# Performance work log

Hardware: AMD Instinct MI355X
Metric: run time of the kernel (lower is better)

The kernel has to match this reference:

```python
import jax, jax.numpy as jnp
import numpy as np

B, CIN, COUT, H, W = 16, 128, 128, 64, 64
E, PS, FF = 8, 16, 8
GC, HID, HC = 4 * FF, 64, COUT * 4  # gate_channel, gate hidden, bottleneck hidden


def conv(x, w, stride=1, pad=0, groups=1):
    # x: [B,C,H,W], w: [O,I/groups,kh,kw]
    return jax.lax.conv_general_dilated(
        x, w, (stride, stride), [(pad, pad), (pad, pad)], feature_group_count=groups)


def group_norm(x, scale, bias, groups, eps=1e-5):
    b, c = x.shape[:2]
    xr = x.reshape(b, groups, c // groups, *x.shape[2:])
    m = xr.mean(axis=(2, 3, 4), keepdims=True)
    v = xr.var(axis=(2, 3, 4), keepdims=True)
    xr = (xr - m) * jax.lax.rsqrt(v + eps)
    return xr.reshape(x.shape) * scale[None, :, None, None] + bias[None, :, None, None]


def setup_inputs() -> dict:
    key = jax.random.key(0)
    ks = jax.random.split(key, 8)
    f = lambda k, shp: jax.random.normal(k, shp, jnp.float32) * 0.05
    return dict(
        x=jax.random.normal(ks[0], (B, CIN, H, W), jnp.float32),
        w_exp=f(ks[1], (E, COUT, CIN, 3, 3)),
        gn_exp_s=jnp.ones((E, COUT), jnp.float32),
        gn_exp_b=jnp.zeros((E, COUT), jnp.float32),
        w1=f(ks[2], (GC, HID)), b1=jnp.zeros((HID,), jnp.float32),
        w2=f(ks[3], (HID, E)), b2=jnp.zeros((E,), jnp.float32),
        w_pw1=f(ks[4], (HC, COUT, 1, 1)),
        gn1_s=jnp.ones((HC,), jnp.float32), gn1_b=jnp.zeros((HC,), jnp.float32),
        w_dw=f(ks[5], (HC, 1, 3, 3)),
        gn2_s=jnp.ones((HC,), jnp.float32), gn2_b=jnp.zeros((HC,), jnp.float32),
        w_pw2=f(ks[6], (COUT, HC, 1, 1)),
        gn3_s=jnp.ones((COUT,), jnp.float32), gn3_b=jnp.zeros((COUT,), jnp.float32),
    )


def reference(x, w_exp, gn_exp_s, gn_exp_b, w1, b1, w2, b2,
              w_pw1, gn1_s, gn1_b, w_dw, gn2_s, gn2_b, w_pw2, gn3_s, gn3_b):
    # ---- Conv experts (residual 3x3 conv + GN + SiLU), vmapped over experts ----
    def expert(w, s, b):
        y = conv(x, w, pad=1)
        y = group_norm(y, s, b, groups=min(8, COUT))
        return jax.nn.silu(y) + x  # use_residual=True, CIN == COUT

    ys = jax.vmap(expert)(w_exp, gn_exp_s, gn_exp_b)  # [E,B,C,H,W]

    # ---- Router gate: Fourier features of patch-center coordinates ----
    ph, pw = H // PS, W // PS
    cy = (jnp.arange(ph, dtype=jnp.float32) + 0.5) / ph
    cx = (jnp.arange(pw, dtype=jnp.float32) + 0.5) / pw
    freqs = (2.0 ** jnp.arange(FF, dtype=jnp.float32)) * jnp.pi
    ay = cy[:, None] * freqs  # [ph,FF]
    ax = cx[:, None] * freqs  # [pw,FF]
    feats = jnp.concatenate([
        jnp.broadcast_to(jnp.sin(ay)[:, None, :], (ph, pw, FF)),
        jnp.broadcast_to(jnp.cos(ay)[:, None, :], (ph, pw, FF)),
        jnp.broadcast_to(jnp.sin(ax)[None, :, :], (ph, pw, FF)),
        jnp.broadcast_to(jnp.cos(ax)[None, :, :], (ph, pw, FF)),
    ], axis=-1)  # [ph,pw,4*FF] == gate_channel
    hgate = jax.nn.silu(feats @ w1 + b1)
    wts = jax.nn.softmax(hgate @ w2 + b2, axis=-1)  # [ph,pw,E]

    # ---- Patch-wise combine of expert outputs ----
    wmap = jnp.repeat(jnp.repeat(wts, PS, axis=0), PS, axis=1)  # [H,W,E]
    combined = jnp.einsum('ebchw,hwe->bchw', ys, wmap)

    # ---- Inverted bottleneck: 1x1 -> dw3x3 -> 1x1(stride2) with GN+SiLU ----
    h = jax.nn.silu(group_norm(conv(combined, w_pw1), gn1_s, gn1_b, groups=8))
    h = jax.nn.silu(group_norm(conv(h, w_dw, pad=1, groups=HC), gn2_s, gn2_b, groups=8))
    h = jax.nn.silu(group_norm(conv(h, w_pw2, stride=2), gn3_s, gn3_b, groups=8))
    return h  # [B, COUT, H//2, W//2]
```

## Files before the change

kernel.cpp:

```cpp
#include <hip/hip_runtime.h>
#include <hip/hip_bf16.h>


#define B_ 16
#define CIN_ 128
#define COUT_ 128
#define H_ 64
#define W_ 64
#define HW_ 4096
#define E_ 8
#define FF_ 8
#define GC_ 32
#define HID_ 64
#define HC_ 512

typedef __hip_bfloat16 bf16;
typedef __bf16 bf16x8 __attribute__((ext_vector_type(8)));
typedef float f32x4 __attribute__((ext_vector_type(4)));
typedef float f32x16 __attribute__((ext_vector_type(16)));

__device__ __forceinline__ float siluf(float v) { return v / (1.f + __expf(-v)); }
__device__ __forceinline__ float bf2f(bf16 v) { return __bfloat162float(v); }
__device__ __forceinline__ bf16 f2bf(float v) { return __float2bfloat16(v); }

__device__ __forceinline__ void async16(void* lds, const void* g) {
  __builtin_amdgcn_global_load_lds(
      (const __attribute__((address_space(1))) unsigned int*)g,
      (__attribute__((address_space(3))) unsigned int*)lds, 16, 0, 0);
}

__global__ void gate_kernel(const float* __restrict__ w1, const float* __restrict__ b1,
                            const float* __restrict__ w2, const float* __restrict__ b2,
                            float* __restrict__ wts) {
  int p = threadIdx.x;
  if (p >= 16) return;
  int i = p >> 2, j = p & 3;
  float cy = (i + 0.5f) * 0.25f;
  float cx = (j + 0.5f) * 0.25f;
  float feats[GC_];
#pragma unroll
  for (int f = 0; f < FF_; ++f) {
    float fr = 3.14159265358979f * (float)(1 << f);
    float ay = cy * fr, ax = cx * fr;
    feats[f] = sinf(ay);
    feats[FF_ + f] = cosf(ay);
    feats[2 * FF_ + f] = sinf(ax);
    feats[3 * FF_ + f] = cosf(ax);
  }
  float hid[HID_];
  for (int k = 0; k < HID_; ++k) {
    float a = b1[k];
#pragma unroll
    for (int m = 0; m < GC_; ++m) a = fmaf(feats[m], w1[m * HID_ + k], a);
    hid[k] = siluf(a);
  }
  float lg[E_];
  float mx = -1e30f;
#pragma unroll
  for (int e = 0; e < E_; ++e) {
    float a = b2[e];
    for (int k = 0; k < HID_; ++k) a = fmaf(hid[k], w2[k * E_ + e], a);
    lg[e] = a;
    mx = fmaxf(mx, a);
  }
  float s = 0.f;
#pragma unroll
  for (int e = 0; e < E_; ++e) { lg[e] = __expf(lg[e] - mx); s += lg[e]; }
  float inv = 1.f / s;
#pragma unroll
  for (int e = 0; e < E_; ++e) wts[p * E_ + e] = lg[e] * inv;
}

__global__ __launch_bounds__(256) void xt_kernel(const float* __restrict__ x,
                                                 bf16* __restrict__ xT) {
  __shared__ float t[128][65];
  int b = blockIdx.x >> 6, h = blockIdx.x & 63;
  int tid = threadIdx.x;
  int w = tid & 63, c4 = tid >> 6;
  const float* xb = x + ((size_t)(b * 128) * 64 + h) * 64;
#pragma unroll 4
  for (int rep = 0; rep < 32; ++rep) {
    int ci = rep * 4 + c4;
    t[ci][w] = xb[(size_t)ci * HW_ + w];
  }
  __syncthreads();
  bf16* dst = xT + (size_t)(b * 64 + h) * 8192;
#pragma unroll 4
  for (int rep = 0; rep < 32; ++rep) {
    int o = rep * 256 + tid;
    int cg = o >> 9, w2 = (o >> 3) & 63, lo = o & 7;
    dst[o] = f2bf(t[cg * 8 + lo][w2]);
  }
}

__global__ void wt_kernel(const float* __restrict__ w_exp, bf16* __restrict__ wT) {
  int idx = blockIdx.x * 256 + threadIdx.x;
  if (idx >= 1179648) return;
  int lo = idx & 7;
  int co = (idx >> 3) & 127;
  int cg = (idx >> 10) & 15;
  int rest = idx >> 14;
  int tap = rest % 9, e = rest / 9;
  int ci = cg * 8 + lo;
  wT[idx] = f2bf(w_exp[(((size_t)(e * 128 + co) * 128 + ci) * 9) + tap]);
}

__global__ void wpT_kernel(const float* __restrict__ w_pw1, const float* __restrict__ w_pw2,
                           bf16* __restrict__ wp1T, bf16* __restrict__ wp2T) {
  int idx = blockIdx.x * 256 + threadIdx.x;
  if (idx < 65536) wp1T[idx] = f2bf(w_pw1[idx]);
  else if (idx < 131072) wp2T[idx - 65536] = f2bf(w_pw2[idx - 65536]);
}

__global__ __launch_bounds__(256, 2) void conv_mfma(
    const bf16* __restrict__ xT, const bf16* __restrict__ wT,
    float* __restrict__ statsE, bf16* __restrict__ ys) {
  __shared__ __align__(16) char xls[4 * 6336];
  __shared__ __align__(16) char wls[2][3 * 8192];
  __shared__ float red[4][8][2];

  int blk = blockIdx.x;
  int xcd = blk & 7;
  int r2 = blk >> 3;
  int b = xcd * 2 + (r2 & 1);
  int rest = r2 >> 1;
  int rt = rest & 15, e = rest >> 4;

  int tid = threadIdx.x, lane = tid & 63, wave = tid >> 6;
  int hi = lane >> 5, l31 = lane & 31;
  int h0 = rt * 4;

  if (tid < 48) {
    int cg = tid / 12, rem = tid % 12;
    int r = rem >> 1, edge = rem & 1;
    *(uint4*)(xls + cg * 6336 + r * 1056 + edge * 1040) = make_uint4(0u, 0u, 0u, 0u);
  }
  int rbad = (rt == 0) ? 0 : (rt == 15 ? 5 : -1);
  if (rbad >= 0) {
    int cg = tid >> 6, slot = (tid & 63) + 1;
    *(uint4*)(xls + cg * 6336 + rbad * 1056 + slot * 16) = make_uint4(0u, 0u, 0u, 0u);
  }

  f32x16 acc[4][2];
#pragma unroll
  for (int mt = 0; mt < 4; ++mt)
#pragma unroll
    for (int nt = 0; nt < 2; ++nt)
#pragma unroll
      for (int r = 0; r < 16; ++r) acc[mt][nt][r] = 0.f;

  for (int q = 0; q < 4; ++q) {
    if (q) __syncthreads();
    {
      int cg = wave;
#pragma unroll
      for (int r = 0; r < 6; ++r) {
        int h = h0 - 1 + r;
        if ((unsigned)h < 64u) {
          const char* g = (const char*)xT +
              ((size_t)((b * 64 + h) * 16) + q * 4 + cg) * 1024 + lane * 16;
          async16(xls + cg * 6336 + r * 1056 + 16, g);
        }
      }
    }
#pragma unroll
    for (int s = 0; s < 6; ++s) {
      int seg = wave * 6 + s;
      int tap = seg >> 3, rem = seg & 7;
      int cg = rem >> 1, cb = rem & 1;
      const char* g = (const char*)wT +
          ((size_t)(((e * 9 + tap) * 16) + q * 4 + cg) * 128 + cb * 64) * 16 + lane * 16;
      async16(wls[0] + (tap * 4 + cg) * 2048 + cb * 1024, g);
    }
    __syncthreads();

    for (int dr = 0; dr < 3; ++dr) {
      int buf = dr & 1;
      if (dr < 2) {
#pragma unroll
        for (int s = 0; s < 6; ++s) {
          int seg = wave * 6 + s;
          int tap = seg >> 3, rem = seg & 7;
          int cg = rem >> 1, cb = rem & 1;
          const char* g = (const char*)wT +
              ((size_t)(((e * 9 + (dr + 1) * 3 + tap) * 16) + q * 4 + cg) * 128 + cb * 64) * 16 +
              lane * 16;
          async16(wls[buf ^ 1] + (tap * 4 + cg) * 2048 + cb * 1024, g);
        }
      }
      int r_local = wave + dr;
      const char* wb = wls[buf];
      const char* xrow = xls;
      bf16x8 afp[2][2], bfp[2][2];
      {
        int cgl = hi;
        afp[0][0] = *(const bf16x8*)(wb + cgl * 2048 + (0 * 32 + l31) * 16);
        afp[0][1] = *(const bf16x8*)(wb + cgl * 2048 + (1 * 32 + l31) * 16);
        const char* xr = xrow + cgl * 6336 + r_local * 1056;
        bfp[0][0] = *(const bf16x8*)(xr + (0 * 32 + l31 + 0) * 16);
        bfp[0][1] = *(const bf16x8*)(xr + (1 * 32 + l31 + 0) * 16);
      }
#pragma unroll
      for (int s = 0; s < 12; ++s) {
        int mh = s & 1;
        int cura = s & 1, curb = (s >> 1) & 1;
        if (s < 11) {
          int s1 = s + 1;
          int ds1 = s1 >> 2, ks1 = (s1 >> 1) & 1, mh1 = s1 & 1;
          int cgl1 = ks1 * 2 + hi;
          const char* wt1 = wb + ds1 * 8192 + cgl1 * 2048;
          afp[s1 & 1][0] = *(const bf16x8*)(wt1 + ((mh1 * 2 + 0) * 32 + l31) * 16);
          afp[s1 & 1][1] = *(const bf16x8*)(wt1 + ((mh1 * 2 + 1) * 32 + l31) * 16);
          if (mh1 == 0) {
            const char* xr1 = xrow + cgl1 * 6336 + r_local * 1056;
            bfp[(s1 >> 1) & 1][0] = *(const bf16x8*)(xr1 + (0 * 32 + l31 + ds1) * 16);
            bfp[(s1 >> 1) & 1][1] = *(const bf16x8*)(xr1 + (1 * 32 + l31 + ds1) * 16);
          }
        }
#pragma unroll
        for (int i = 0; i < 2; ++i)
#pragma unroll
          for (int nt = 0; nt < 2; ++nt)
            acc[mh * 2 + i][nt] = __builtin_amdgcn_mfma_f32_32x32x16_bf16(
                afp[cura][i], bfp[curb][nt], acc[mh * 2 + i][nt], 0, 0, 0);
      }
      if (dr < 2) __syncthreads();
    }
  }

  int hh = h0 + wave;
  bf16* yb = ys + (size_t)((e * 16 + b) * 128) * 4096;
#pragma unroll
  for (int mt = 0; mt < 4; ++mt) {
    float s0 = 0.f, ss0 = 0.f, s1 = 0.f, ss1 = 0.f;
#pragma unroll
    for (int nt = 0; nt < 2; ++nt) {
      int w = nt * 32 + l31;
      int pos = hh * 64 + w;
#pragma unroll
      for (int r = 0; r < 16; ++r) {
        float v = acc[mt][nt][r];
        if (r < 8) { s0 += v; ss0 += v * v; } else { s1 += v; ss1 += v * v; }
        int row = (r & 3) + 8 * (r >> 2) + 4 * hi;
        yb[(size_t)(mt * 32 + row) * 4096 + pos] = f2bf(v);
      }
    }
#pragma unroll
    for (int off = 32; off; off >>= 1) {
      s0 += __shfl_down(s0, off, 64);
      ss0 += __shfl_down(ss0, off, 64);
      s1 += __shfl_down(s1, off, 64);
      ss1 += __shfl_down(ss1, off, 64);
    }
    if (lane == 0) {
      red[wave][mt * 2][0] = s0; red[wave][mt * 2][1] = ss0;
      red[wave][mt * 2 + 1][0] = s1; red[wave][mt * 2 + 1][1] = ss1;
    }
  }
  __syncthreads();
  if (tid < 16) {
    int g = tid >> 1, which = tid & 1;
    float t = red[0][g][which] + red[1][g][which] + red[2][g][which] + red[3][g][which];
    atomicAdd(&statsE[((e * 16 + b) * 8 + g) * 2 + which], t);
  }
}

__global__ __launch_bounds__(256) void combine_cl(
    const float* __restrict__ x, const bf16* __restrict__ ys,
    const float* __restrict__ stE, const float* __restrict__ gns,
    const float* __restrict__ gnb, const float* __restrict__ wts,
    bf16* __restrict__ ccl) {
  __shared__ bf16 tile[64][132];
  int b = blockIdx.x >> 6, h = blockIdx.x & 63;
  int t = threadIdx.x;
  int oct = t & 7, cq = t >> 3;
  int w0 = oct * 8;
  int gidx = cq >> 2;
  int pid = (h >> 4) * 4 + (w0 >> 4);
  int pos = h * 64 + w0;

  float m_[8], r_[8], wt_[8];
#pragma unroll
  for (int e = 0; e < 8; ++e) {
    float S = stE[((e * 16 + b) * 8 + gidx) * 2];
    float SS = stE[((e * 16 + b) * 8 + gidx) * 2 + 1];
    float mean = S * (1.f / 65536.f);
    float var = SS * (1.f / 65536.f) - mean * mean;
    m_[e] = mean;
    r_[e] = rsqrtf(var + 1e-5f);
    wt_[e] = wts[pid * 8 + e];
  }

#pragma unroll
  for (int k = 0; k < 4; ++k) {
    int co = cq * 4 + k;
    const float* xp = x + ((size_t)(b * 128 + co) << 12) + pos;
    float v[8];
    float4 xa = *(const float4*)xp;
    float4 xb2 = *(const float4*)(xp + 4);
    v[0] = xa.x; v[1] = xa.y; v[2] = xa.z; v[3] = xa.w;
    v[4] = xb2.x; v[5] = xb2.y; v[6] = xb2.z; v[7] = xb2.w;
#pragma unroll
    for (int e = 0; e < 8; ++e) {
      uint4 u = *(const uint4*)(ys + ((size_t)((e * 16 + b) * 128 + co) << 12) + pos);
      const bf16* pv = (const bf16*)&u;
      float sc = r_[e] * gns[e * 128 + co];
      float sh = gnb[e * 128 + co] - m_[e] * sc;
#pragma unroll
      for (int j = 0; j < 8; ++j) {
        float yn = bf2f(pv[j]) * sc + sh;
        v[j] = fmaf(siluf(yn), wt_[e], v[j]);
      }
    }
#pragma unroll
    for (int j = 0; j < 8; ++j) tile[w0 + j][co] = f2bf(v[j]);
  }
  __syncthreads();
  int row = t >> 2, q = t & 3;
  char* dst = (char*)ccl + ((size_t)(b * 4096 + h * 64 + row)) * 256 + q * 64;
  const char* src = (const char*)&tile[row][0] + q * 64;
#pragma unroll
  for (int i = 0; i < 4; ++i)
    *(uint4*)(dst + i * 16) = *(const uint4*)(src + i * 16);
}

__global__ __launch_bounds__(256) void pw1_mfma(
    const bf16* __restrict__ ccl, const bf16* __restrict__ wp1T,
    bf16* __restrict__ h1cl, float* __restrict__ stats1) {
  __shared__ __align__(16) char ls[65536];
  __shared__ float red[4][2][2];
  char* als = ls;
  char* bls = ls + 32768;
  int blk = blockIdx.x;
  int ntile = blk & 511, mtile = blk >> 9;
  int n0 = ntile * 128, m0 = mtile * 128;
  int t = threadIdx.x, lane = t & 63, wave = t >> 6;
  int quad = lane >> 4, l15 = lane & 15;
  int b = n0 >> 12;

#pragma unroll
  for (int i = 0; i < 8; ++i) {
    int id = t + 256 * i;
    int r = id >> 4, c = id & 15;
    *(uint4*)(als + c * 2048 + r * 16) =
        *(const uint4*)((const char*)wp1T + (size_t)(m0 + r) * 256 + c * 16);
    *(uint4*)(bls + c * 2048 + r * 16) =
        *(const uint4*)((const char*)ccl + (size_t)(n0 + r) * 256 + c * 16);
  }
  __syncthreads();

  f32x4 acc[8][2];
#pragma unroll
  for (int mt = 0; mt < 8; ++mt)
#pragma unroll
    for (int nt = 0; nt < 2; ++nt) acc[mt][nt] = (f32x4){0.f, 0.f, 0.f, 0.f};

#pragma unroll
  for (int kc = 0; kc < 4; ++kc) {
    int cgq = kc * 4 + quad;
    bf16x8 af[8];
#pragma unroll
    for (int mt = 0; mt < 8; ++mt)
      af[mt] = *(const bf16x8*)(als + cgq * 2048 + (mt * 16 + l15) * 16);
    bf16x8 bfr[2];
#pragma unroll
    for (int nt = 0; nt < 2; ++nt)
      bfr[nt] = *(const bf16x8*)(bls + cgq * 2048 + (wave * 32 + nt * 16 + l15) * 16);
#pragma unroll
    for (int mt = 0; mt < 8; ++mt)
#pragma unroll
      for (int nt = 0; nt < 2; ++nt)
        acc[mt][nt] = __builtin_amdgcn_mfma_f32_16x16x32_bf16(
            af[mt], bfr[nt], acc[mt][nt], 0, 0, 0);
  }

  __syncthreads();
  float s[2] = {0.f, 0.f}, ss[2] = {0.f, 0.f};
  bf16* tile = (bf16*)ls;
#pragma unroll
  for (int mt = 0; mt < 8; ++mt) {
    int gi = mt >> 2;
#pragma unroll
    for (int nt = 0; nt < 2; ++nt) {
      int n = wave * 32 + nt * 16 + l15;
#pragma unroll
      for (int r = 0; r < 4; ++r) {
        float v = acc[mt][nt][r];
        s[gi] += v;
        ss[gi] += v * v;
        tile[n * 132 + mt * 16 + quad * 4 + r] = f2bf(v);
      }
    }
  }
#pragma unroll
  for (int gi = 0; gi < 2; ++gi) {
#pragma unroll
    for (int off = 32; off; off >>= 1) {
      s[gi] += __shfl_down(s[gi], off, 64);
      ss[gi] += __shfl_down(ss[gi], off, 64);
    }
  }
  if (lane == 0) {
    red[wave][0][0] = s[0]; red[wave][0][1] = ss[0];
    red[wave][1][0] = s[1]; red[wave][1][1] = ss[1];
  }
  __syncthreads();
  if (t < 4) {
    int gi = t >> 1, which = t & 1;
    float v = red[0][gi][which] + red[1][gi][which] + red[2][gi][which] + red[3][gi][which];
    atomicAdd(&stats1[(b * 8 + mtile * 2 + gi) * 2 + which], v);
  }
#pragma unroll
  for (int i = 0; i < 8; ++i) {
    int id = t + 256 * i;
    int r = id >> 4, q = id & 15;
    char* dst = (char*)h1cl + (size_t)(n0 + r) * 1024 + m0 * 2 + q * 16;
    const char* src = (const char*)tile + r * 264 + q * 16;
    *(uint4*)dst = *(const uint4*)src;
  }
}

__global__ __launch_bounds__(256) void dw_cl(
    const bf16* __restrict__ h1cl, const float* __restrict__ w_dw,
    const float* __restrict__ st1, const float* __restrict__ gs,
    const float* __restrict__ gb, bf16* __restrict__ h2cl,
    float* __restrict__ stats2) {
  __shared__ __align__(16) bf16 tile[18 * 66 * 16];
  __shared__ float red2[4][2];
  int blk = blockIdx.x;
  int ht = blk & 3, hcg = (blk >> 2) & 31, b = blk >> 7;
  int h0 = ht * 16;
  int hc0 = hcg * 16;
  int hcb = hcg >> 2;
  int t = threadIdx.x;

  float S1 = st1[(b * 8 + hcb) * 2], SS1 = st1[(b * 8 + hcb) * 2 + 1];
  float mean = S1 * (1.f / 262144.f);
  float var1 = SS1 * (1.f / 262144.f) - mean * mean;
  float rstd = rsqrtf(var1 + 1e-5f);
  float scale[16], shift[16];
#pragma unroll
  for (int j = 0; j < 16; ++j) {
    float g = gs[hc0 + j];
    scale[j] = rstd * g;
    shift[j] = gb[hc0 + j] - mean * rstd * g;
  }

  for (int i = 0; i < 5; ++i) {
    int idx = t + 256 * i;
    if (idx >= 1188) break;
    int row = idx / 66, wslot = idx - row * 66;
    int hh = h0 - 1 + row;
    int w = wslot - 1;
    int swz = (wslot >> 2) & 3;
    bf16* dst = tile + (row * 66 + wslot) * 16;
    if ((unsigned)hh < 64u && (unsigned)w < 64u) {
      const char* p = (const char*)h1cl + ((size_t)(b * 4096 + hh * 64 + w) * 512 + hc0) * 2;
      uint4 a0 = *(const uint4*)p;
      uint4 a1 = *(const uint4*)(p + 16);
      const bf16* pv = (const bf16*)&a0;
      const bf16* pv1 = (const bf16*)&a1;
      bf16 outv[16];
#pragma unroll
      for (int j = 0; j < 8; ++j)
        outv[j] = f2bf(siluf(bf2f(pv[j]) * scale[j] + shift[j]));
#pragma unroll
      for (int j = 0; j < 8; ++j)
        outv[8 + j] = f2bf(siluf(bf2f(pv1[j]) * scale[8 + j] + shift[8 + j]));
#pragma unroll
      for (int qq = 0; qq < 4; ++qq) {
        int ph = (qq + swz) & 3;
        *(uint2*)(dst + ph * 4) = *(const uint2*)(outv + qq * 4);
      }
    } else {
      *(uint4*)dst = make_uint4(0u, 0u, 0u, 0u);
      *(uint4*)(dst + 8) = make_uint4(0u, 0u, 0u, 0u);
    }
  }
  __syncthreads();

  int w = t & 63, q = t >> 6;
  float wv[9][4];
#pragma unroll
  for (int j = 0; j < 4; ++j) {
    int hc = hc0 + q * 4 + j;
#pragma unroll
    for (int tap = 0; tap < 9; ++tap) wv[tap][j] = w_dw[hc * 9 + tap];
  }

  f32x4 win[3][3];
  float acc_s = 0.f, acc_ss = 0.f;

  auto ld4 = [&](int r, int dwi) -> f32x4 {
    int slot = w + dwi;
    int ph = (q + (slot >> 2)) & 3;
    const bf16* p = tile + (r * 66 + slot) * 16 + ph * 4;
    uint2 u = *(const uint2*)p;
    const bf16* pb = (const bf16*)&u;
    return (f32x4){bf2f(pb[0]), bf2f(pb[1]), bf2f(pb[2]), bf2f(pb[3])};
  };

#pragma unroll
  for (int dwi = 0; dwi < 3; ++dwi) {
    win[0][dwi] = ld4(0, dwi);
    win[1][dwi] = ld4(1, dwi);
  }
#pragma unroll
  for (int orow = 0; orow < 16; ++orow) {
    int rnew = orow + 2;
    int ringn = rnew % 3;
#pragma unroll
    for (int dwi = 0; dwi < 3; ++dwi) win[ringn][dwi] = ld4(rnew, dwi);
    f32x4 acc = (f32x4){0.f, 0.f, 0.f, 0.f};
#pragma unroll
    for (int dr = 0; dr < 3; ++dr) {
      int ring = (orow + dr) % 3;
#pragma unroll
      for (int dwi = 0; dwi < 3; ++dwi) {
#pragma unroll
        for (int j = 0; j < 4; ++j)
          acc[j] = fmaf(win[ring][dwi][j], wv[dr * 3 + dwi][j], acc[j]);
      }
    }
#pragma unroll
    for (int j = 0; j < 4; ++j) { acc_s += acc[j]; acc_ss += acc[j] * acc[j]; }
    if (!(orow & 1) && !(w & 1)) {
      int hglob = h0 + orow;
      int pos2 = (hglob >> 1) * 32 + (w >> 1);
      bf16 tmp[4];
#pragma unroll
      for (int j = 0; j < 4; ++j) tmp[j] = f2bf(acc[j]);
      *(uint2*)((char*)h2cl + ((size_t)(b * 1024 + pos2) * 512 + hc0 + q * 4) * 2) =
          *(const uint2*)tmp;
    }
  }

#pragma unroll
  for (int off = 32; off; off >>= 1) {
    acc_s += __shfl_down(acc_s, off, 64);
    acc_ss += __shfl_down(acc_ss, off, 64);
  }
  int wave = t >> 6;
  if ((t & 63) == 0) { red2[wave][0] = acc_s; red2[wave][1] = acc_ss; }
  __syncthreads();
  if (t < 2) {
    float v = red2[0][t] + red2[1][t] + red2[2][t] + red2[3][t];
    atomicAdd(&stats2[(b * 8 + hcb) * 2 + t], v);
  }
}

__global__ __launch_bounds__(256) void pw2_mfma(
    const bf16* __restrict__ h2, const bf16* __restrict__ wp2T,
    const float* __restrict__ st2, const float* __restrict__ gs2,
    const float* __restrict__ gb2, float* __restrict__ h3,
    float* __restrict__ stats3) {
  __shared__ __align__(16) char als[2][8192];
  __shared__ __align__(16) char bls[2][4096];
  __shared__ float red[4][8][2];
  int blk = blockIdx.x;
  int n0 = blk * 64;
  int b = n0 >> 10, posb = n0 & 1023;
  int t = threadIdx.x, lane = t & 63, wave = t >> 6;
  int quad = lane >> 4, l15 = lane & 15;
  int wbase = wave * 16;
  int c4 = t >> 6, r = t & 63;

  auto load_bls = [&](char* dst, int kc) {
    int hc0 = (kc * 4 + c4) * 8;
    int g = hc0 >> 6;
    float S = st2[(b * 8 + g) * 2], SS = st2[(b * 8 + g) * 2 + 1];
    float mean = S * (1.f / 262144.f);
    float rstd = rsqrtf(SS * (1.f / 262144.f) - mean * mean + 1e-5f);
    uint4 u = *(const uint4*)((const char*)h2 + (size_t)(n0 + r) * 1024 +
                              (size_t)(kc * 4 + c4) * 16);
    const bf16* pv = (const bf16*)&u;
    bf16 outv[8];
#pragma unroll
    for (int j = 0; j < 8; ++j) {
      float xv = bf2f(pv[j]);
      xv = (xv - mean) * rstd * gs2[hc0 + j] + gb2[hc0 + j];
      outv[j] = f2bf(siluf(xv));
    }
    *(uint4*)dst = *(const uint4*)outv;
  };

  f32x4 acc[8];
#pragma unroll
  for (int mt = 0; mt < 8; ++mt) acc[mt] = (f32x4){0.f, 0.f, 0.f, 0.f};

  {
#pragma unroll
    for (int i = 0; i < 2; ++i) {
      int id = t + 256 * i;
      int cc = id >> 7, rr = id & 127;
      *(uint4*)(als[0] + cc * 2048 + rr * 16) =
          *(const uint4*)((const char*)wp2T + (size_t)rr * 1024 + cc * 16);
    }
    load_bls(bls[0] + c4 * 1024 + r * 16, 0);
  }
#pragma unroll
  for (int kc = 0; kc < 16; ++kc) {
    __syncthreads();
    if (kc + 1 < 16) {
      int nb = (kc + 1) & 1;
#pragma unroll
      for (int i = 0; i < 2; ++i) {
        int id = t + 256 * i;
        int cc = id >> 7, rr = id & 127;
        *(uint4*)(als[nb] + cc * 2048 + rr * 16) =
            *(const uint4*)((const char*)wp2T + (size_t)rr * 1024 + ((kc + 1) * 4 + cc) * 16);
      }
      load_bls(bls[nb] + c4 * 1024 + r * 16, kc + 1);
    }
    int buf = kc & 1;
    bf16x8 bf1 = *(const bf16x8*)(bls[buf] + quad * 1024 + (wbase + l15) * 16);
#pragma unroll
    for (int mt = 0; mt < 8; ++mt) {
      bf16x8 af = *(const bf16x8*)(als[buf] + quad * 2048 + (mt * 16 + l15) * 16);
      acc[mt] = __builtin_amdgcn_mfma_f32_16x16x32_bf16(af, bf1, acc[mt], 0, 0, 0);
    }
  }

#pragma unroll
  for (int mt = 0; mt < 8; ++mt) {
    float s = 0.f, ss = 0.f;
    int pos = posb + wbase + l15;
#pragma unroll
    for (int rr = 0; rr < 4; ++rr) {
      float v = acc[mt][rr];
      s += v;
      ss += v * v;
      int co = mt * 16 + quad * 4 + rr;
      h3[(size_t)(b * 128 + co) * 1024 + pos] = v;
    }
#pragma unroll
    for (int off = 32; off; off >>= 1) {
      s += __shfl_down(s, off, 64);
      ss += __shfl_down(ss, off, 64);
    }
    if (lane == 0) { red[wave][mt][0] = s; red[wave][mt][1] = ss; }
  }
  __syncthreads();
  if (t < 16) {
    int mt = t >> 1, which = t & 1;
    float v = red[0][mt][which] + red[1][mt][which] + red[2][mt][which] + red[3][mt][which];
    atomicAdd(&stats3[(b * 8 + mt) * 2 + which], v);
  }
}

__global__ void out_kernel(const float* __restrict__ h3, const float* __restrict__ stats,
                           const float* __restrict__ gs, const float* __restrict__ gb,
                           float* __restrict__ out) {
  const int total = B_ * COUT_ * 1024;
  for (int idx = blockIdx.x * blockDim.x + threadIdx.x; idx < total; idx += gridDim.x * blockDim.x) {
    int c = (idx >> 10) & 127;
    int b = idx >> 17;
    int bg = b * 8 + (c >> 4);
    float S = stats[bg * 2], SS = stats[bg * 2 + 1];
    float mean = S * (1.f / 16384.f);
    float var = SS * (1.f / 16384.f) - mean * mean;
    float rstd = rsqrtf(var + 1e-5f);
    float v = (h3[idx] - mean) * rstd * gs[c] + gb[c];
    out[idx] = siluf(v);
  }
}

extern "C" void kernel_launch(void* const* d_in, const int* in_sizes, int n_in,
                              void* d_out, int out_size, void* d_ws, size_t ws_size,
                              hipStream_t stream) {
  const float* x = (const float*)d_in[0];
  const float* w_exp = (const float*)d_in[1];
  const float* gn_exp_s = (const float*)d_in[2];
  const float* gn_exp_b = (const float*)d_in[3];
  const float* w1 = (const float*)d_in[4];
  const float* b1 = (const float*)d_in[5];
  const float* w2 = (const float*)d_in[6];
  const float* b2 = (const float*)d_in[7];
  const float* w_pw1 = (const float*)d_in[8];
  const float* gn1_s = (const float*)d_in[9];
  const float* gn1_b = (const float*)d_in[10];
  const float* w_dw = (const float*)d_in[11];
  const float* gn2_s = (const float*)d_in[12];
  const float* gn2_b = (const float*)d_in[13];
  const float* w_pw2 = (const float*)d_in[14];
  const float* gn3_s = (const float*)d_in[15];
  const float* gn3_b = (const float*)d_in[16];

  char* ws = (char*)d_ws;
  const size_t WP1T_OFF = 16384;
  const size_t WP2T_OFF = WP1T_OFF + 131072;
  const size_t XT_OFF = WP2T_OFF + 131072;
  const size_t WT_OFF = XT_OFF + 16777216;
  const size_t YS_OFF = WT_OFF + 2359296;
  const size_t NEEDED = YS_OFF + 134217728;
  if (ws_size < NEEDED) return;

  float* wts = (float*)ws;
  float* stats1 = (float*)(ws + 1024);
  float* stats2 = (float*)(ws + 2048);
  float* stats3 = (float*)(ws + 3072);
  float* statsE = (float*)(ws + 4096);
  bf16* wp1T = (bf16*)(ws + WP1T_OFF);
  bf16* wp2T = (bf16*)(ws + WP2T_OFF);
  bf16* xT = (bf16*)(ws + XT_OFF);
  bf16* ccl = (bf16*)(ws + XT_OFF);
  bf16* wT = (bf16*)(ws + WT_OFF);
  bf16* ys = (bf16*)(ws + YS_OFF);
  bf16* h1cl = (bf16*)(ws + YS_OFF);
  bf16* h2cl = (bf16*)(ws + YS_OFF + 67108864);
  float* h3 = (float*)(ws + YS_OFF + 83886080);

  hipMemsetAsync(ws, 0, 16384, stream);
  gate_kernel<<<1, 64, 0, stream>>>(w1, b1, w2, b2, wts);
  xt_kernel<<<B_ * 64, 256, 0, stream>>>(x, xT);
  wt_kernel<<<4608, 256, 0, stream>>>(w_exp, wT);
  wpT_kernel<<<512, 256, 0, stream>>>(w_pw1, w_pw2, wp1T, wp2T);
  conv_mfma<<<E_ * B_ * 16, 256, 0, stream>>>(xT, wT, statsE, ys);
  combine_cl<<<B_ * 64, 256, 0, stream>>>(x, ys, statsE, gn_exp_s, gn_exp_b, wts, ccl);
  pw1_mfma<<<4 * 512, 256, 0, stream>>>(ccl, wp1T, h1cl, stats1);
  dw_cl<<<B_ * 32 * 4, 256, 0, stream>>>(h1cl, w_dw, stats1, gn1_s, gn1_b, h2cl, stats2);
  pw2_mfma<<<256, 256, 0, stream>>>(h2cl, wp2T, stats2, gn2_s, gn2_b, h3, stats3);
  out_kernel<<<1024, 256, 0, stream>>>(h3, stats3, gn3_s, gn3_b, (float*)d_out);
}
```

Measured before the change: 481.7 us.

## Shrink expert conv tiles to two rows and split output channels across waves

The expert 3x3 conv kernel now processes two output rows per block instead of four, with waves split 2x2 over rows and output-channel halves. Each wave holds half as many accumulators. The double-buffered weight LDS is replaced by a single buffer with extra barriers, and the launch bound is raised to three blocks per CU. The aim is higher occupancy and lower register/LDS pressure. In exchange, the software prefetch of weights and fragments is lost, each block reuses its loaded weights over fewer rows, and the halo overhead per row rises.

Measured after the change: 512.2 us. 6.3% more time.

```diff
diff --git a/kernel.cpp b/kernel.cpp
--- a/kernel.cpp
+++ b/kernel.cpp
@@ -112,38 +112,45 @@
   else if (idx < 131072) wp2T[idx - 65536] = f2bf(w_pw2[idx - 65536]);
 }
 
-__global__ __launch_bounds__(256, 2) void conv_mfma(
+__global__ __launch_bounds__(256, 3) void conv_mfma(
     const bf16* __restrict__ xT, const bf16* __restrict__ wT,
     float* __restrict__ statsE, bf16* __restrict__ ys) {
-  __shared__ __align__(16) char xls[4 * 6336];
-  __shared__ __align__(16) char wls[2][3 * 8192];
-  __shared__ float red[4][8][2];
+  __shared__ __align__(16) char xls[4 * 4224];
+  __shared__ __align__(16) char wls[3 * 8192];
+  __shared__ float red[4][4][2];
 
   int blk = blockIdx.x;
   int xcd = blk & 7;
   int r2 = blk >> 3;
   int b = xcd * 2 + (r2 & 1);
   int rest = r2 >> 1;
-  int rt = rest & 15, e = rest >> 4;
+  int rp = rest & 31, e = rest >> 5;
 
   int tid = threadIdx.x, lane = tid & 63, wave = tid >> 6;
   int hi = lane >> 5, l31 = lane & 31;
-  int h0 = rt * 4;
-
-  if (tid < 48) {
-    int cg = tid / 12, rem = tid % 12;
+  int wr = wave & 1, wm = wave >> 1;
+  int h0 = rp * 2;
+
+  if (tid < 32) {
+    int cg = tid >> 3, rem = tid & 7;
     int r = rem >> 1, edge = rem & 1;
-    *(uint4*)(xls + cg * 6336 + r * 1056 + edge * 1040) = make_uint4(0u, 0u, 0u, 0u);
-  }
-  int rbad = (rt == 0) ? 0 : (rt == 15 ? 5 : -1);
+    *(uint4*)(xls + cg * 4224 + r * 1056 + edge * 1040) = make_uint4(0u, 0u, 0u, 0u);
+  }
+  int rbad = (rp == 0) ? 0 : (rp == 31 ? 3 : -1);
   if (rbad >= 0) {
-    int cg = tid >> 6, slot = (tid & 63) + 1;
-    *(uint4*)(xls + cg * 6336 + rbad * 1056 + slot * 16) = make_uint4(0u, 0u, 0u, 0u);
-  }
-
-  f32x16 acc[4][2];
-#pragma unroll
-  for (int mt = 0; mt < 4; ++mt)
+#pragma unroll
+    for (int i = 0; i < 2; ++i) {
+      int idx = tid + 256 * i;
+      if (idx < 264) {
+        int cg = idx / 66, slot = idx - cg * 66;
+        *(uint4*)(xls + cg * 4224 + rbad * 1056 + slot * 16) = make_uint4(0u, 0u, 0u, 0u);
+      }
+    }
+  }
+
+  f32x16 acc[2][2];
+#pragma unroll
+  for (int mt = 0; mt < 2; ++mt)
 #pragma unroll
     for (int nt = 0; nt < 2; ++nt)
 #pragma unroll
@@ -154,84 +161,73 @@
     {
       int cg = wave;
 #pragma unroll
-      for (int r = 0; r < 6; ++r) {
+      for (int r = 0; r < 4; ++r) {
         int h = h0 - 1 + r;
         if ((unsigned)h < 64u) {
           const char* g = (const char*)xT +
               ((size_t)((b * 64 + h) * 16) + q * 4 + cg) * 1024 + lane * 16;
-          async16(xls + cg * 6336 + r * 1056 + 16, g);
+          async16(xls + cg * 4224 + r * 1056 + 16, g);
         }
       }
     }
 #pragma unroll
     for (int s = 0; s < 6; ++s) {
       int seg = wave * 6 + s;
-      int tap = seg >> 3, rem = seg & 7;
+      int ts = seg >> 3, rem = seg & 7;
       int cg = rem >> 1, cb = rem & 1;
       const char* g = (const char*)wT +
-          ((size_t)(((e * 9 + tap) * 16) + q * 4 + cg) * 128 + cb * 64) * 16 + lane * 16;
-      async16(wls[0] + (tap * 4 + cg) * 2048 + cb * 1024, g);
+          ((size_t)(((e * 9 + ts) * 16) + q * 4 + cg) * 128 + cb * 64) * 16 + lane * 16;
+      async16(wls + (ts * 4 + cg) * 2048 + cb * 1024, g);
     }
     __syncthreads();
 
     for (int dr = 0; dr < 3; ++dr) {
-      int buf = dr & 1;
+      int r_local = wr + dr;
+      __builtin_amdgcn_s_setprio(1);
+#pragma unroll
+      for (int ds = 0; ds < 3; ++ds) {
+#pragma unroll
+        for (int ks = 0; ks < 2; ++ks) {
+          int cgl = ks * 2 + hi;
+          bf16x8 af[2], bfr[2];
+#pragma unroll
+          for (int mt = 0; mt < 2; ++mt)
+            af[mt] = *(const bf16x8*)(wls + (ds * 4 + cgl) * 2048 +
+                                      (wm * 64 + mt * 32 + l31) * 16);
+#pragma unroll
+          for (int nt = 0; nt < 2; ++nt)
+            bfr[nt] = *(const bf16x8*)(xls + cgl * 4224 + r_local * 1056 +
+                                       (nt * 32 + l31 + ds) * 16);
+#pragma unroll
+          for (int mt = 0; mt < 2; ++mt)
+#pragma unroll
+            for (int nt = 0; nt < 2; ++nt)
+              acc[mt][nt] = __builtin_amdgcn_mfma_f32_32x32x16_bf16(
+                  af[mt], bfr[nt], acc[mt][nt], 0, 0, 0);
+        }
+      }
+      __builtin_amdgcn_s_setprio(0);
       if (dr < 2) {
+        __syncthreads();
 #pragma unroll
         for (int s = 0; s < 6; ++s) {
           int seg = wave * 6 + s;
-          int tap = seg >> 3, rem = seg & 7;
+          int ts = seg >> 3, rem = seg & 7;
           int cg = rem >> 1, cb = rem & 1;
           const char* g = (const char*)wT +
-              ((size_t)(((e * 9 + (dr + 1) * 3 + tap) * 16) + q * 4 + cg) * 128 + cb * 64) * 16 +
+              ((size_t)(((e * 9 + (dr + 1) * 3 + ts) * 16) + q * 4 + cg) * 128 + cb * 64) * 16 +
               lane * 16;
-          async16(wls[buf ^ 1] + (tap * 4 + cg) * 2048 + cb * 1024, g);
+          async16(wls + (ts * 4 + cg) * 2048 + cb * 1024, g);
         }
-      }
-      int r_local = wave + dr;
-      const char* wb = wls[buf];
-      const char* xrow = xls;
-      bf16x8 afp[2][2], bfp[2][2];
-      {
-        int cgl = hi;
-        afp[0][0] = *(const bf16x8*)(wb + cgl * 2048 + (0 * 32 + l31) * 16);
-        afp[0][1] = *(const bf16x8*)(wb + cgl * 2048 + (1 * 32 + l31) * 16);
-        const char* xr = xrow + cgl * 6336 + r_local * 1056;
-        bfp[0][0] = *(const bf16x8*)(xr + (0 * 32 + l31 + 0) * 16);
-        bfp[0][1] = *(const bf16x8*)(xr + (1 * 32 + l31 + 0) * 16);
-      }
-#pragma unroll
-      for (int s = 0; s < 12; ++s) {
-        int mh = s & 1;
-        int cura = s & 1, curb = (s >> 1) & 1;
-        if (s < 11) {
-          int s1 = s + 1;
-          int ds1 = s1 >> 2, ks1 = (s1 >> 1) & 1, mh1 = s1 & 1;
-          int cgl1 = ks1 * 2 + hi;
-          const char* wt1 = wb + ds1 * 8192 + cgl1 * 2048;
-          afp[s1 & 1][0] = *(const bf16x8*)(wt1 + ((mh1 * 2 + 0) * 32 + l31) * 16);
-          afp[s1 & 1][1] = *(const bf16x8*)(wt1 + ((mh1 * 2 + 1) * 32 + l31) * 16);
-          if (mh1 == 0) {
-            const char* xr1 = xrow + cgl1 * 6336 + r_local * 1056;
-            bfp[(s1 >> 1) & 1][0] = *(const bf16x8*)(xr1 + (0 * 32 + l31 + ds1) * 16);
-            bfp[(s1 >> 1) & 1][1] = *(const bf16x8*)(xr1 + (1 * 32 + l31 + ds1) * 16);
-          }
-        }
-#pragma unroll
-        for (int i = 0; i < 2; ++i)
-#pragma unroll
-          for (int nt = 0; nt < 2; ++nt)
-            acc[mh * 2 + i][nt] = __builtin_amdgcn_mfma_f32_32x32x16_bf16(
-                afp[cura][i], bfp[curb][nt], acc[mh * 2 + i][nt], 0, 0, 0);
-      }
-      if (dr < 2) __syncthreads();
-    }
-  }
-
-  int hh = h0 + wave;
+        __syncthreads();
+      }
+    }
+  }
+
+  int hh = h0 + wr;
   bf16* yb = ys + (size_t)((e * 16 + b) * 128) * 4096;
 #pragma unroll
-  for (int mt = 0; mt < 4; ++mt) {
+  for (int mt = 0; mt < 2; ++mt) {
     float s0 = 0.f, ss0 = 0.f, s1 = 0.f, ss1 = 0.f;
 #pragma unroll
     for (int nt = 0; nt < 2; ++nt) {
@@ -242,7 +238,7 @@
         float v = acc[mt][nt][r];
         if (r < 8) { s0 += v; ss0 += v * v; } else { s1 += v; ss1 += v * v; }
         int row = (r & 3) + 8 * (r >> 2) + 4 * hi;
-        yb[(size_t)(mt * 32 + row) * 4096 + pos] = f2bf(v);
+        yb[(size_t)(wm * 64 + mt * 32 + row) * 4096 + pos] = f2bf(v);
       }
     }
 #pragma unroll
@@ -260,7 +256,8 @@
   __syncthreads();
   if (tid < 16) {
     int g = tid >> 1, which = tid & 1;
-    float t = red[0][g][which] + red[1][g][which] + red[2][g][which] + red[3][g][which];
+    int wmg = g >> 2, sub = g & 3;
+    float t = red[wmg * 2][sub][which] + red[wmg * 2 + 1][sub][which];
     atomicAdd(&statsE[((e * 16 + b) * 8 + g) * 2 + which], t);
   }
 }
@@ -715,7 +712,7 @@
   xt_kernel<<<B_ * 64, 256, 0, stream>>>(x, xT);
   wt_kernel<<<4608, 256, 0, stream>>>(w_exp, wT);
   wpT_kernel<<<512, 256, 0, stream>>>(w_pw1, w_pw2, wp1T, wp2T);
-  conv_mfma<<<E_ * B_ * 16, 256, 0, stream>>>(xT, wT, statsE, ys);
+  conv_mfma<<<4096, 256, 0, stream>>>(xT, wT, statsE, ys);
   combine_cl<<<B_ * 64, 256, 0, stream>>>(x, ys, statsE, gn_exp_s, gn_exp_b, wts, ccl);
   pw1_mfma<<<4 * 512, 256, 0, stream>>>(ccl, wp1T, h1cl, stats1);
   dw_cl<<<B_ * 32 * 4, 256, 0, stream>>>(h1cl, w_dw, stats1, gn1_s, gn1_b, h2cl, stats2);
```
